# Optimization experiments

Measured on AMD Instinct MI355X. Metric: run time of the kernel, lower is better.

The kernel has to match this reference:

```python
import jax, jax.numpy as jnp
import numpy as np
import math

PHI = (1 + math.sqrt(5)) / 2
TABLE_SIZE = 4096
TWO_PI = 2.0 * math.pi
_ang = np.arange(TABLE_SIZE, dtype=np.float32) * (TWO_PI / TABLE_SIZE)
SIN_T = jnp.asarray(np.sin(_ang))
COS_T = jnp.asarray(np.cos(_ang))


def lookup_sin_cos(theta):
    """LUT sin/cos with linear interpolation over a 4096-entry table on [0, 2pi)."""
    pos = (theta / TWO_PI % 1.0) * TABLE_SIZE
    i0f = jnp.floor(pos)
    frac = pos - i0f
    i0 = i0f.astype(jnp.int32) % TABLE_SIZE
    i1 = (i0 + 1) % TABLE_SIZE
    s = SIN_T[i0] * (1.0 - frac) + SIN_T[i1] * frac
    c = COS_T[i0] * (1.0 - frac) + COS_T[i1] * frac
    return s, c


def setup_inputs() -> dict:
    key = jax.random.key(0)
    ks = jax.random.split(key, 8)
    B, S, D, H = 2, 2048, 1024, 16
    dh = D // H
    return {
        "x": jax.random.normal(ks[0], (B, S, D), dtype=jnp.float32),
        "w_q": jax.random.normal(ks[1], (H, dh), dtype=jnp.float32) * 0.02,
        "b_q": jnp.zeros((H, dh), jnp.float32),
        "phi_q": jnp.full((H, dh), PHI, jnp.float32),
        "w_k": jax.random.normal(ks[2], (H, dh), dtype=jnp.float32) * 0.02,
        "b_k": jnp.zeros((H, dh), jnp.float32),
        "phi_k": jnp.full((H, dh), PHI, jnp.float32),
        "w_v": jax.random.normal(ks[3], (H, dh), dtype=jnp.float32) * 0.02,
        "b_v": jnp.zeros((H, dh), jnp.float32),
        "w_out": jax.random.normal(ks[4], (D,), dtype=jnp.float32) * 0.02,
        "b_out": jnp.zeros((D,), jnp.float32),
    }


def reference(x, w_q, b_q, phi_q, w_k, b_k, phi_k, w_v, b_v, w_out, b_out):
    B, S, D = x.shape
    H, dh = w_q.shape
    scale = math.sqrt(2 * dh)
    t = jnp.arange(S, dtype=x.dtype).reshape(1, S, 1, 1)
    xh = x.reshape(B, S, H, dh)

    theta_q = xh / (1.0 + jnp.abs(w_q)) + b_q + t * phi_q
    sin_q, cos_q = lookup_sin_cos(theta_q)
    Q = jnp.concatenate([cos_q, sin_q], axis=-1)  # (B,S,H,2dh)

    theta_k = xh / (1.0 + jnp.abs(w_k)) + b_k + t * phi_k
    sin_k, cos_k = lookup_sin_cos(theta_k)
    K = jnp.concatenate([cos_k, sin_k], axis=-1)  # (B,S,H,2dh)

    theta_v = xh / (1.0 + jnp.abs(w_v)) + b_v
    sin_v, cos_v = lookup_sin_cos(theta_v)
    V = cos_v + sin_v  # (B,S,H,dh)

    scores = jnp.einsum('bqhd,bkhd->bhqk', Q, K) / scale
    causal = jnp.triu(jnp.ones((S, S), dtype=bool), k=1)
    scores = jnp.where(causal, -jnp.inf, scores)
    attn = jax.nn.softmax(scores, axis=-1)
    out = jnp.einsum('bhqk,bkhd->bqhd', attn, V).reshape(B, S, D)

    theta_out = out / (1.0 + jnp.abs(w_out)) + b_out
    sin_o, cos_o = lookup_sin_cos(theta_out)
    return cos_o + sin_o
```

## Files before the change

### kernel.cpp

```cpp
#include <hip/hip_runtime.h>
#include <hip/hip_bf16.h>
#include <math.h>

#define BB 2
#define SS 2048
#define HH 16
#define DH 64
#define DQK 128
#define DD (HH*DH)
#define QS2   0.12751758f
#define EBIAS 11.5415605f

typedef _Float16 half8_t __attribute__((ext_vector_type(8)));
typedef _Float16 half4_t __attribute__((ext_vector_type(4)));
typedef float f32x4_t __attribute__((ext_vector_type(4)));
typedef float f32x4v __attribute__((ext_vector_type(4)));

__device__ __forceinline__ void fsincos(float th, float* sn, float* cs) {
  float rev = th * 0.15915494309189535f;
  rev -= floorf(rev);
  float ang = rev * 6.283185307179586f;
  *sn = __sinf(ang);
  *cs = __cosf(ang);
}

__device__ __forceinline__ void dma16(const void* g, void* l) {
  __builtin_amdgcn_global_load_lds(
      (const __attribute__((address_space(1))) unsigned int*)g,
      (__attribute__((address_space(3))) unsigned int*)l, 16, 0, 0);
}

__global__ __launch_bounds__(256) void gen_qkv(
    const float* __restrict__ x,
    const float* __restrict__ wq, const float* __restrict__ bq,
    const float* __restrict__ phq,
    const float* __restrict__ wk, const float* __restrict__ bk,
    const float* __restrict__ phk,
    const float* __restrict__ wv, const float* __restrict__ bv,
    _Float16* __restrict__ Qd, _Float16* __restrict__ Kd, _Float16* __restrict__ Vtd)
{
  int stile = blockIdx.x & 31;
  int bh    = blockIdx.x >> 5;
  int b = bh >> 4, h = bh & 15;
  int t = threadIdx.x;
  int sl = t >> 2;
  int dq = (t & 3) << 4;
  int s  = stile * 64 + sl;

  __shared__ _Float16 Vl[64 * 65];

  const float* xr = x + (((size_t)b * SS + s) * HH + h) * DH + dq;
  float xv[16];
#pragma unroll
  for (int i = 0; i < 4; i++)
    *(f32x4v*)(&xv[i * 4]) = *(const f32x4v*)(xr + i * 4);

  float tv = (float)s;
  _Float16 qc[16], qs[16], kc[16], ks[16];
#pragma unroll
  for (int i = 0; i < 16; i++) {
    int d = dq + i;
    int hd = h * DH + d;
    {
      float th = xv[i] / (1.f + fabsf(wq[hd])) + bq[hd] + tv * phq[hd];
      float sn, cs; fsincos(th, &sn, &cs);
      qc[i] = (_Float16)(cs * QS2);
      qs[i] = (_Float16)(sn * QS2);
    }
    {
      float th = xv[i] / (1.f + fabsf(wk[hd])) + bk[hd] + tv * phk[hd];
      float sn, cs; fsincos(th, &sn, &cs);
      kc[i] = (_Float16)cs;
      ks[i] = (_Float16)sn;
    }
    {
      float th = xv[i] / (1.f + fabsf(wv[hd])) + bv[hd];
      float sn, cs; fsincos(th, &sn, &cs);
      Vl[d * 65 + sl] = (_Float16)(cs + sn);
    }
  }
  size_t qbase = ((size_t)bh * SS + s) * DQK;
#pragma unroll
  for (int i = 0; i < 2; i++) {
    *(half8_t*)(Qd + qbase + dq + i * 8)      = *(half8_t*)(&qc[i * 8]);
    *(half8_t*)(Qd + qbase + DH + dq + i * 8) = *(half8_t*)(&qs[i * 8]);
  }
  {
    size_t ktb = ((size_t)bh * 32 + stile) * 8192;
    int fo0 = (t & 3) * 2;
    *(half8_t*)(Kd + ktb + ((size_t)(fo0    ) * 64 + sl) * 8) = *(half8_t*)(&kc[0]);
    *(half8_t*)(Kd + ktb + ((size_t)(fo0 + 1) * 64 + sl) * 8) = *(half8_t*)(&kc[8]);
    *(half8_t*)(Kd + ktb + ((size_t)(fo0 + 8) * 64 + sl) * 8) = *(half8_t*)(&ks[0]);
    *(half8_t*)(Kd + ktb + ((size_t)(fo0 + 9) * 64 + sl) * 8) = *(half8_t*)(&ks[8]);
  }
  __syncthreads();
#pragma unroll
  for (int i = 0; i < 2; i++) {
    int u = t * 2 + i;
    int dv = u & 63, ku = u >> 6;
    _Float16 tmp[8];
#pragma unroll
    for (int jj = 0; jj < 8; jj++) tmp[jj] = Vl[dv * 65 + ku * 8 + jj];
    *(half8_t*)(Vtd + (((size_t)bh * 32 + stile) * 8 + ku) * 512 + dv * 8) =
        *(half8_t*)tmp;
  }
}

__global__ __launch_bounds__(256) void flash_attn(
    const _Float16* __restrict__ Qd, const _Float16* __restrict__ Kd,
    const _Float16* __restrict__ Vtd,
    const float* __restrict__ wout, const float* __restrict__ bout,
    float* __restrict__ out)
{
  int qt = 31 - (blockIdx.x >> 5);
  int bh = blockIdx.x & 31;
  int b  = bh >> 4, hh = bh & 15;
  int nch = qt + 1;
  int q0 = qt * 64;
  int wave = threadIdx.x >> 6;
  int lane = threadIdx.x & 63;
  int lm = lane & 15, lq = lane >> 4;
  int qh = wave >> 1;
  int kh = wave & 1;

  __shared__ __align__(16) _Float16 KV[2][12288];

  const _Float16* Kg = Kd + (size_t)bh * 32 * 8192;
  const _Float16* Vg = Vtd + (size_t)bh * 32 * 4096;

  {
#pragma unroll
    for (int i = 0; i < 4; i++)
      dma16(Kg + (size_t)(wave * 4 + i) * 512 + lane * 8, &KV[0][(wave * 4 + i) * 512]);
#pragma unroll
    for (int i = 0; i < 2; i++)
      dma16(Vg + (size_t)(wave * 2 + i) * 512 + lane * 8, &KV[0][8192 + (wave * 2 + i) * 512]);
  }

  const _Float16* Qb = Qd + ((size_t)bh * SS + q0 + qh * 32) * DQK;
  half8_t aq[2][4];
#pragma unroll
  for (int qtl = 0; qtl < 2; qtl++)
#pragma unroll
    for (int c = 0; c < 4; c++)
      aq[qtl][c] = *(const half8_t*)(Qb + (qtl * 16 + lm) * DQK + c * 32 + lq * 8);

  f32x4_t o[4][2];
  float l[2] = {0.f, 0.f};
#pragma unroll
  for (int dt = 0; dt < 4; dt++)
#pragma unroll
    for (int qtl = 0; qtl < 2; qtl++) o[dt][qtl] = (f32x4_t){0.f, 0.f, 0.f, 0.f};

  const f32x4_t cinit = (f32x4_t){-EBIAS, -EBIAS, -EBIAS, -EBIAS};

  for (int kt = 0; kt < nch; ++kt) {
    int bf = kt & 1;
    __syncthreads();
    if (kt + 1 < nch) {
      int nb = (kt + 1) & 1;
      const _Float16* gK = Kg + (size_t)(kt + 1) * 8192;
      const _Float16* gV = Vg + (size_t)(kt + 1) * 4096;
#pragma unroll
      for (int i = 0; i < 4; i++)
        dma16(gK + (size_t)(wave * 4 + i) * 512 + lane * 8, &KV[nb][(wave * 4 + i) * 512]);
#pragma unroll
      for (int i = 0; i < 2; i++)
        dma16(gV + (size_t)(wave * 2 + i) * 512 + lane * 8, &KV[nb][8192 + (wave * 2 + i) * 512]);
    }

    const _Float16* lK = &KV[bf][0];
    const _Float16* lV = &KV[bf][8192];
    int k0 = kt * 64;

    f32x4_t cST[2][2];
    cST[0][0] = cST[0][1] = cST[1][0] = cST[1][1] = cinit;
#pragma unroll
    for (int c = 0; c < 4; c++) {
      half8_t k0f = *(const half8_t*)(lK + ((size_t)(c * 4 + lq) * 64 + kh * 32 + lm) * 8);
      half8_t k1f = *(const half8_t*)(lK + ((size_t)(c * 4 + lq) * 64 + kh * 32 + 16 + lm) * 8);
      cST[0][0] = __builtin_amdgcn_mfma_f32_16x16x32_f16(k0f, aq[0][c], cST[0][0], 0, 0, 0);
      cST[0][1] = __builtin_amdgcn_mfma_f32_16x16x32_f16(k0f, aq[1][c], cST[0][1], 0, 0, 0);
      cST[1][0] = __builtin_amdgcn_mfma_f32_16x16x32_f16(k1f, aq[0][c], cST[1][0], 0, 0, 0);
      cST[1][1] = __builtin_amdgcn_mfma_f32_16x16x32_f16(k1f, aq[1][c], cST[1][1], 0, 0, 0);
    }

    bool maskit = (kt == nch - 1);
    half4_t pb[2][2];
#pragma unroll
    for (int ktl = 0; ktl < 2; ktl++)
#pragma unroll
      for (int qtl = 0; qtl < 2; qtl++) {
        float pf[4];
#pragma unroll
        for (int r = 0; r < 4; r++) {
          float sv = cST[ktl][qtl][r];
          if (maskit) {
            int key  = k0 + kh * 32 + ktl * 16 + lq * 4 + r;
            int qrow = q0 + qh * 32 + qtl * 16 + lm;
            if (key > qrow) sv = -1e30f;
          }
          pf[r] = __builtin_exp2f(sv);
          l[qtl] += pf[r];
        }
        pb[ktl][qtl] = (half4_t){(_Float16)pf[0], (_Float16)pf[1],
                                 (_Float16)pf[2], (_Float16)pf[3]};
      }

#pragma unroll
    for (int dt = 0; dt < 4; dt++)
#pragma unroll
      for (int kg = 0; kg < 2; kg++) {
        half4_t vf = *(const half4_t*)(lV +
            ((size_t)(kh * 4 + kg * 2 + (lq >> 1)) * 64 + dt * 16 + lm) * 8 + (lq & 1) * 4);
        o[dt][0] = __builtin_amdgcn_mfma_f32_16x16x16f16(vf, pb[kg][0], o[dt][0], 0, 0, 0);
        o[dt][1] = __builtin_amdgcn_mfma_f32_16x16x16f16(vf, pb[kg][1], o[dt][1], 0, 0, 0);
      }
  }

#pragma unroll
  for (int qtl = 0; qtl < 2; qtl++) {
    l[qtl] += __shfl_xor(l[qtl], 16);
    l[qtl] += __shfl_xor(l[qtl], 32);
  }

  int sc = nch & 1;
  float* Of = (float*)&KV[sc][0];
  float* Lf = Of + 64 * 68;
  __syncthreads();
  if (kh == 1) {
#pragma unroll
    for (int qtl = 0; qtl < 2; qtl++) {
      int row = qh * 32 + qtl * 16 + lm;
#pragma unroll
      for (int dt = 0; dt < 4; dt++)
#pragma unroll
        for (int r = 0; r < 4; r++)
          Of[row * 68 + dt * 16 + lq * 4 + r] = o[dt][qtl][r];
      if (lq == 0) Lf[row] = l[qtl];
    }
  }
  __syncthreads();
  if (kh == 0) {
#pragma unroll
    for (int qtl = 0; qtl < 2; qtl++) {
      int row = qh * 32 + qtl * 16 + lm;
      float rl = 1.f / (l[qtl] + Lf[row]);
#pragma unroll
      for (int dt = 0; dt < 4; dt++)
#pragma unroll
        for (int r = 0; r < 4; r++) {
          int idx = row * 68 + dt * 16 + lq * 4 + r;
          Of[idx] = (o[dt][qtl][r] + Of[idx]) * rl;
        }
    }
  }
  __syncthreads();
  {
    int dcol = hh * DH + lane;
    float iw = 1.f / (1.f + fabsf(wout[dcol]));
    float bo = bout[dcol];
#pragma unroll
    for (int rr = 0; rr < 16; rr++) {
      int row = wave * 16 + rr;
      float th = Of[row * 68 + lane] * iw + bo;
      float sn, cs; fsincos(th, &sn, &cs);
      out[((size_t)b * SS + q0 + row) * DD + dcol] = cs + sn;
    }
  }
}

extern "C" void kernel_launch(void* const* d_in, const int* in_sizes, int n_in,
                              void* d_out, int out_size, void* d_ws, size_t ws_size,
                              hipStream_t stream) {
  (void)in_sizes; (void)n_in; (void)out_size; (void)ws_size;
  const float* x   = (const float*)d_in[0];
  const float* wq  = (const float*)d_in[1];
  const float* bq  = (const float*)d_in[2];
  const float* phq = (const float*)d_in[3];
  const float* wk  = (const float*)d_in[4];
  const float* bk  = (const float*)d_in[5];
  const float* phk = (const float*)d_in[6];
  const float* wv  = (const float*)d_in[7];
  const float* bv  = (const float*)d_in[8];
  const float* wo  = (const float*)d_in[9];
  const float* bo  = (const float*)d_in[10];

  _Float16* Qd  = (_Float16*)d_ws;
  _Float16* Kd  = Qd + (size_t)BB * HH * SS * DQK;
  _Float16* Vtd = Kd + (size_t)BB * HH * SS * DQK;

  gen_qkv<<<BB * HH * (SS / 64), 256, 0, stream>>>(
      x, wq, bq, phq, wk, bk, phk, wv, bv, Qd, Kd, Vtd);
  flash_attn<<<32 * 32, 256, 0, stream>>>(
      Qd, Kd, Vtd, wo, bo, (float*)d_out);
}
```

Measured before the change: 141.5 us.

## Load V fragments directly from global, rebalance tile order, hoist per-dim weights

The attention kernel stops staging V through LDS and reads V fragments straight from global memory into registers each chunk, which shrinks shared memory and allows a min-blocks launch bound of 4. Query tiles are reordered in interleaved long/short tiers to balance causal work across CUs. Wave priority is raised around MFMA sections, P conversion uses packed RTZ conversion, and the epilogue uses a transposed LDS layout with fast reciprocals. The QKV generator hoists weight loads into vector loads and replaces divisions with reciprocals. Direct global V reads add latency that is not prefetched and may stall the PV MFMAs.

```diff
diff --git a/kernel.cpp b/kernel.cpp
--- a/kernel.cpp
+++ b/kernel.cpp
@@ -13,6 +13,7 @@
 
 typedef _Float16 half8_t __attribute__((ext_vector_type(8)));
 typedef _Float16 half4_t __attribute__((ext_vector_type(4)));
+typedef __fp16  fp16x2_t __attribute__((ext_vector_type(2)));
 typedef float f32x4_t __attribute__((ext_vector_type(4)));
 typedef float f32x4v __attribute__((ext_vector_type(4)));
 
@@ -55,26 +56,57 @@
   for (int i = 0; i < 4; i++)
     *(f32x4v*)(&xv[i * 4]) = *(const f32x4v*)(xr + i * 4);
 
+  int hd0 = h * DH + dq;
+  float iwqv[16], vbq[16], vpq[16];
+  float iwkv[16], vbk[16], vpk[16];
+  float iwvv[16], vbv[16];
+#pragma unroll
+  for (int i = 0; i < 4; i++) {
+    f32x4v w4, b4, p4;
+    w4 = *(const f32x4v*)(wq + hd0 + i * 4);
+    b4 = *(const f32x4v*)(bq + hd0 + i * 4);
+    p4 = *(const f32x4v*)(phq + hd0 + i * 4);
+#pragma unroll
+    for (int j = 0; j < 4; j++) {
+      iwqv[i*4+j] = __builtin_amdgcn_rcpf(1.f + fabsf(w4[j]));
+      vbq[i*4+j] = b4[j]; vpq[i*4+j] = p4[j];
+    }
+    w4 = *(const f32x4v*)(wk + hd0 + i * 4);
+    b4 = *(const f32x4v*)(bk + hd0 + i * 4);
+    p4 = *(const f32x4v*)(phk + hd0 + i * 4);
+#pragma unroll
+    for (int j = 0; j < 4; j++) {
+      iwkv[i*4+j] = __builtin_amdgcn_rcpf(1.f + fabsf(w4[j]));
+      vbk[i*4+j] = b4[j]; vpk[i*4+j] = p4[j];
+    }
+    w4 = *(const f32x4v*)(wv + hd0 + i * 4);
+    b4 = *(const f32x4v*)(bv + hd0 + i * 4);
+#pragma unroll
+    for (int j = 0; j < 4; j++) {
+      iwvv[i*4+j] = __builtin_amdgcn_rcpf(1.f + fabsf(w4[j]));
+      vbv[i*4+j] = b4[j];
+    }
+  }
+
   float tv = (float)s;
   _Float16 qc[16], qs[16], kc[16], ks[16];
 #pragma unroll
   for (int i = 0; i < 16; i++) {
     int d = dq + i;
-    int hd = h * DH + d;
     {
-      float th = xv[i] / (1.f + fabsf(wq[hd])) + bq[hd] + tv * phq[hd];
+      float th = xv[i] * iwqv[i] + vbq[i] + tv * vpq[i];
       float sn, cs; fsincos(th, &sn, &cs);
       qc[i] = (_Float16)(cs * QS2);
       qs[i] = (_Float16)(sn * QS2);
     }
     {
-      float th = xv[i] / (1.f + fabsf(wk[hd])) + bk[hd] + tv * phk[hd];
+      float th = xv[i] * iwkv[i] + vbk[i] + tv * vpk[i];
       float sn, cs; fsincos(th, &sn, &cs);
       kc[i] = (_Float16)cs;
       ks[i] = (_Float16)sn;
     }
     {
-      float th = xv[i] / (1.f + fabsf(wv[hd])) + bv[hd];
+      float th = xv[i] * iwvv[i] + vbv[i];
       float sn, cs; fsincos(th, &sn, &cs);
       Vl[d * 65 + sl] = (_Float16)(cs + sn);
     }
@@ -106,16 +138,19 @@
   }
 }
 
-__global__ __launch_bounds__(256) void flash_attn(
+__global__ __launch_bounds__(256, 4) void flash_attn(
     const _Float16* __restrict__ Qd, const _Float16* __restrict__ Kd,
     const _Float16* __restrict__ Vtd,
     const float* __restrict__ wout, const float* __restrict__ bout,
     float* __restrict__ out)
 {
-  int qt = 31 - (blockIdx.x >> 5);
+  int g  = blockIdx.x >> 5;
   int bh = blockIdx.x & 31;
+  int r8 = g & 7, tier = g >> 3;
+  int nch = (tier == 0) ? 32 - r8 : (tier == 1) ? 1 + r8
+          : (tier == 2) ? 24 - r8 : 9 + r8;
+  int qt = nch - 1;
   int b  = bh >> 4, hh = bh & 15;
-  int nch = qt + 1;
   int q0 = qt * 64;
   int wave = threadIdx.x >> 6;
   int lane = threadIdx.x & 63;
@@ -123,7 +158,7 @@
   int qh = wave >> 1;
   int kh = wave & 1;
 
-  __shared__ __align__(16) _Float16 KV[2][12288];
+  __shared__ __align__(16) _Float16 KV[2][8192];
 
   const _Float16* Kg = Kd + (size_t)bh * 32 * 8192;
   const _Float16* Vg = Vtd + (size_t)bh * 32 * 4096;
@@ -132,9 +167,6 @@
 #pragma unroll
     for (int i = 0; i < 4; i++)
       dma16(Kg + (size_t)(wave * 4 + i) * 512 + lane * 8, &KV[0][(wave * 4 + i) * 512]);
-#pragma unroll
-    for (int i = 0; i < 2; i++)
-      dma16(Vg + (size_t)(wave * 2 + i) * 512 + lane * 8, &KV[0][8192 + (wave * 2 + i) * 512]);
   }
 
   const _Float16* Qb = Qd + ((size_t)bh * SS + q0 + qh * 32) * DQK;
@@ -153,6 +185,8 @@
     for (int qtl = 0; qtl < 2; qtl++) o[dt][qtl] = (f32x4_t){0.f, 0.f, 0.f, 0.f};
 
   const f32x4_t cinit = (f32x4_t){-EBIAS, -EBIAS, -EBIAS, -EBIAS};
+
+  const _Float16* vbase = Vg + ((size_t)(kh * 4 + (lq >> 1)) * 64 + lm) * 8 + (lq & 1) * 4;
 
   for (int kt = 0; kt < nch; ++kt) {
     int bf = kt & 1;
@@ -160,21 +194,17 @@
     if (kt + 1 < nch) {
       int nb = (kt + 1) & 1;
       const _Float16* gK = Kg + (size_t)(kt + 1) * 8192;
-      const _Float16* gV = Vg + (size_t)(kt + 1) * 4096;
 #pragma unroll
       for (int i = 0; i < 4; i++)
         dma16(gK + (size_t)(wave * 4 + i) * 512 + lane * 8, &KV[nb][(wave * 4 + i) * 512]);
-#pragma unroll
-      for (int i = 0; i < 2; i++)
-        dma16(gV + (size_t)(wave * 2 + i) * 512 + lane * 8, &KV[nb][8192 + (wave * 2 + i) * 512]);
     }
 
     const _Float16* lK = &KV[bf][0];
-    const _Float16* lV = &KV[bf][8192];
     int k0 = kt * 64;
 
     f32x4_t cST[2][2];
     cST[0][0] = cST[0][1] = cST[1][0] = cST[1][1] = cinit;
+    __builtin_amdgcn_s_setprio(1);
 #pragma unroll
     for (int c = 0; c < 4; c++) {
       half8_t k0f = *(const half8_t*)(lK + ((size_t)(c * 4 + lq) * 64 + kh * 32 + lm) * 8);
@@ -184,6 +214,15 @@
       cST[1][0] = __builtin_amdgcn_mfma_f32_16x16x32_f16(k1f, aq[0][c], cST[1][0], 0, 0, 0);
       cST[1][1] = __builtin_amdgcn_mfma_f32_16x16x32_f16(k1f, aq[1][c], cST[1][1], 0, 0, 0);
     }
+    __builtin_amdgcn_s_setprio(0);
+
+    const _Float16* gV = vbase + (size_t)kt * 4096;
+    half4_t vfr[4][2];
+#pragma unroll
+    for (int dt = 0; dt < 4; dt++)
+#pragma unroll
+      for (int kg = 0; kg < 2; kg++)
+        vfr[dt][kg] = *(const half4_t*)(gV + kg * 1024 + dt * 128);
 
     bool maskit = (kt == nch - 1);
     half4_t pb[2][2];
@@ -203,19 +242,21 @@
           pf[r] = __builtin_exp2f(sv);
           l[qtl] += pf[r];
         }
-        pb[ktl][qtl] = (half4_t){(_Float16)pf[0], (_Float16)pf[1],
-                                 (_Float16)pf[2], (_Float16)pf[3]};
+        fp16x2_t h01 = __builtin_amdgcn_cvt_pkrtz(pf[0], pf[1]);
+        fp16x2_t h23 = __builtin_amdgcn_cvt_pkrtz(pf[2], pf[3]);
+        pb[ktl][qtl] = (half4_t){(_Float16)h01.x, (_Float16)h01.y,
+                                 (_Float16)h23.x, (_Float16)h23.y};
       }
 
+    __builtin_amdgcn_s_setprio(1);
 #pragma unroll
     for (int dt = 0; dt < 4; dt++)
 #pragma unroll
       for (int kg = 0; kg < 2; kg++) {
-        half4_t vf = *(const half4_t*)(lV +
-            ((size_t)(kh * 4 + kg * 2 + (lq >> 1)) * 64 + dt * 16 + lm) * 8 + (lq & 1) * 4);
-        o[dt][0] = __builtin_amdgcn_mfma_f32_16x16x16f16(vf, pb[kg][0], o[dt][0], 0, 0, 0);
-        o[dt][1] = __builtin_amdgcn_mfma_f32_16x16x16f16(vf, pb[kg][1], o[dt][1], 0, 0, 0);
+        o[dt][0] = __builtin_amdgcn_mfma_f32_16x16x16f16(vfr[dt][kg], pb[kg][0], o[dt][0], 0, 0, 0);
+        o[dt][1] = __builtin_amdgcn_mfma_f32_16x16x16f16(vfr[dt][kg], pb[kg][1], o[dt][1], 0, 0, 0);
       }
+    __builtin_amdgcn_s_setprio(0);
   }
 
 #pragma unroll
@@ -224,9 +265,8 @@
     l[qtl] += __shfl_xor(l[qtl], 32);
   }
 
-  int sc = nch & 1;
-  float* Of = (float*)&KV[sc][0];
-  float* Lf = Of + 64 * 68;
+  float* Ot = (float*)&KV[0][0];
+  float* Lf = Ot + 64 * 67;
   __syncthreads();
   if (kh == 1) {
 #pragma unroll
@@ -235,8 +275,8 @@
 #pragma unroll
       for (int dt = 0; dt < 4; dt++)
 #pragma unroll
-        for (int r = 0; r < 4; r++)
-          Of[row * 68 + dt * 16 + lq * 4 + r] = o[dt][qtl][r];
+        for (int rr = 0; rr < 4; rr++)
+          Ot[(dt * 16 + lq * 4 + rr) * 67 + row] = o[dt][qtl][rr];
       if (lq == 0) Lf[row] = l[qtl];
     }
   }
@@ -245,25 +285,25 @@
 #pragma unroll
     for (int qtl = 0; qtl < 2; qtl++) {
       int row = qh * 32 + qtl * 16 + lm;
-      float rl = 1.f / (l[qtl] + Lf[row]);
+      float rl = __builtin_amdgcn_rcpf(l[qtl] + Lf[row]);
 #pragma unroll
       for (int dt = 0; dt < 4; dt++)
 #pragma unroll
-        for (int r = 0; r < 4; r++) {
-          int idx = row * 68 + dt * 16 + lq * 4 + r;
-          Of[idx] = (o[dt][qtl][r] + Of[idx]) * rl;
+        for (int rr = 0; rr < 4; rr++) {
+          int idx = (dt * 16 + lq * 4 + rr) * 67 + row;
+          Ot[idx] = (o[dt][qtl][rr] + Ot[idx]) * rl;
         }
     }
   }
   __syncthreads();
   {
     int dcol = hh * DH + lane;
-    float iw = 1.f / (1.f + fabsf(wout[dcol]));
+    float iw = __builtin_amdgcn_rcpf(1.f + fabsf(wout[dcol]));
     float bo = bout[dcol];
 #pragma unroll
     for (int rr = 0; rr < 16; rr++) {
       int row = wave * 16 + rr;
-      float th = Of[row * 68 + lane] * iw + bo;
+      float th = Ot[lane * 67 + row] * iw + bo;
       float sn, cs; fsincos(th, &sn, &cs);
       out[((size_t)b * SS + q0 + row) * DD + dcol] = cs + sn;
     }
```

Measured after the change: 143.5 us. About the same (+1.4%).

## Use hardware revolution-based sin/cos, fold cos+sin into one sine, hoist params, set MFMA priority

Applied to the files above, without the earlier changes.

The sincos helper now feeds the normalized revolution value directly to the hardware sin/cos builtins, which take revolutions, so the multiply back by 2π goes away. Terms of the form cos+sin become sqrt(2)*sin(x+π/4), which needs one transcendental instead of two. Per-dimension weights are loaded as vectors with a reciprocal hoisted out of the loop instead of dividing per element, and s_setprio brackets the MFMA sections of the attention loop. The single-sine identity and the approximate reciprocal change rounding slightly.

```diff
diff --git a/kernel.cpp b/kernel.cpp
--- a/kernel.cpp
+++ b/kernel.cpp
@@ -19,9 +19,13 @@
 __device__ __forceinline__ void fsincos(float th, float* sn, float* cs) {
   float rev = th * 0.15915494309189535f;
   rev -= floorf(rev);
-  float ang = rev * 6.283185307179586f;
-  *sn = __sinf(ang);
-  *cs = __cosf(ang);
+  *sn = __builtin_amdgcn_sinf(rev);
+  *cs = __builtin_amdgcn_cosf(rev);
+}
+__device__ __forceinline__ float fsc_sum(float th) {
+  float rev = th * 0.15915494309189535f + 0.125f;
+  rev -= floorf(rev);
+  return 1.41421356237f * __builtin_amdgcn_sinf(rev);
 }
 
 __device__ __forceinline__ void dma16(const void* g, void* l) {
@@ -55,28 +59,58 @@
   for (int i = 0; i < 4; i++)
     *(f32x4v*)(&xv[i * 4]) = *(const f32x4v*)(xr + i * 4);
 
+  int hd0 = h * DH + dq;
+  float iwqv[16], vbq[16], vpq[16];
+  float iwkv[16], vbk[16], vpk[16];
+  float iwvv[16], vbv[16];
+#pragma unroll
+  for (int i = 0; i < 4; i++) {
+    f32x4v w4, b4, p4;
+    w4 = *(const f32x4v*)(wq + hd0 + i * 4);
+    b4 = *(const f32x4v*)(bq + hd0 + i * 4);
+    p4 = *(const f32x4v*)(phq + hd0 + i * 4);
+#pragma unroll
+    for (int j = 0; j < 4; j++) {
+      iwqv[i*4+j] = __builtin_amdgcn_rcpf(1.f + fabsf(w4[j]));
+      vbq[i*4+j] = b4[j]; vpq[i*4+j] = p4[j];
+    }
+    w4 = *(const f32x4v*)(wk + hd0 + i * 4);
+    b4 = *(const f32x4v*)(bk + hd0 + i * 4);
+    p4 = *(const f32x4v*)(phk + hd0 + i * 4);
+#pragma unroll
+    for (int j = 0; j < 4; j++) {
+      iwkv[i*4+j] = __builtin_amdgcn_rcpf(1.f + fabsf(w4[j]));
+      vbk[i*4+j] = b4[j]; vpk[i*4+j] = p4[j];
+    }
+    w4 = *(const f32x4v*)(wv + hd0 + i * 4);
+    b4 = *(const f32x4v*)(bv + hd0 + i * 4);
+#pragma unroll
+    for (int j = 0; j < 4; j++) {
+      iwvv[i*4+j] = __builtin_amdgcn_rcpf(1.f + fabsf(w4[j]));
+      vbv[i*4+j] = b4[j];
+    }
+  }
+
   float tv = (float)s;
   _Float16 qc[16], qs[16], kc[16], ks[16];
 #pragma unroll
   for (int i = 0; i < 16; i++) {
     int d = dq + i;
-    int hd = h * DH + d;
     {
-      float th = xv[i] / (1.f + fabsf(wq[hd])) + bq[hd] + tv * phq[hd];
+      float th = xv[i] * iwqv[i] + vbq[i] + tv * vpq[i];
       float sn, cs; fsincos(th, &sn, &cs);
       qc[i] = (_Float16)(cs * QS2);
       qs[i] = (_Float16)(sn * QS2);
     }
     {
-      float th = xv[i] / (1.f + fabsf(wk[hd])) + bk[hd] + tv * phk[hd];
+      float th = xv[i] * iwkv[i] + vbk[i] + tv * vpk[i];
       float sn, cs; fsincos(th, &sn, &cs);
       kc[i] = (_Float16)cs;
       ks[i] = (_Float16)sn;
     }
     {
-      float th = xv[i] / (1.f + fabsf(wv[hd])) + bv[hd];
-      float sn, cs; fsincos(th, &sn, &cs);
-      Vl[d * 65 + sl] = (_Float16)(cs + sn);
+      float th = xv[i] * iwvv[i] + vbv[i];
+      Vl[d * 65 + sl] = (_Float16)fsc_sum(th);
     }
   }
   size_t qbase = ((size_t)bh * SS + s) * DQK;
@@ -175,6 +209,7 @@
 
     f32x4_t cST[2][2];
     cST[0][0] = cST[0][1] = cST[1][0] = cST[1][1] = cinit;
+    __builtin_amdgcn_s_setprio(1);
 #pragma unroll
     for (int c = 0; c < 4; c++) {
       half8_t k0f = *(const half8_t*)(lK + ((size_t)(c * 4 + lq) * 64 + kh * 32 + lm) * 8);
@@ -184,6 +219,7 @@
       cST[1][0] = __builtin_amdgcn_mfma_f32_16x16x32_f16(k1f, aq[0][c], cST[1][0], 0, 0, 0);
       cST[1][1] = __builtin_amdgcn_mfma_f32_16x16x32_f16(k1f, aq[1][c], cST[1][1], 0, 0, 0);
     }
+    __builtin_amdgcn_s_setprio(0);
 
     bool maskit = (kt == nch - 1);
     half4_t pb[2][2];
@@ -207,6 +243,7 @@
                                  (_Float16)pf[2], (_Float16)pf[3]};
       }
 
+    __builtin_amdgcn_s_setprio(1);
 #pragma unroll
     for (int dt = 0; dt < 4; dt++)
 #pragma unroll
@@ -216,6 +253,7 @@
         o[dt][0] = __builtin_amdgcn_mfma_f32_16x16x16f16(vf, pb[kg][0], o[dt][0], 0, 0, 0);
         o[dt][1] = __builtin_amdgcn_mfma_f32_16x16x16f16(vf, pb[kg][1], o[dt][1], 0, 0, 0);
       }
+    __builtin_amdgcn_s_setprio(0);
   }
 
 #pragma unroll
@@ -264,8 +302,7 @@
     for (int rr = 0; rr < 16; rr++) {
       int row = wave * 16 + rr;
       float th = Of[row * 68 + lane] * iw + bo;
-      float sn, cs; fsincos(th, &sn, &cs);
-      out[((size_t)b * SS + q0 + row) * DD + dcol] = cs + sn;
+      out[((size_t)b * SS + q0 + row) * DD + dcol] = fsc_sum(th);
     }
   }
 }
```

New measurement: 140.6 us. About the same (-0.7%).
